# Optimization experiments

Hardware: AMD Instinct MI355X
Metric: run time of the kernel (lower is better)

Reference implementation:

```python
import jax, jax.numpy as jnp
import numpy as np

LEAKY = 0.1


def _leaky(x):
    return jnp.where(x > 0, x, LEAKY * x)


def _weightnet(d_xyz, ws):
    # d_xyz: [B,N,K,3]; ws: list of (w [Cin,Cout], b [Cout]) -> [B,N,K,W]
    h = d_xyz
    for w, b in ws:
        h = jax.nn.relu(jnp.einsum('bnki,io->bnko', h, w) + b)
    return h


def _gather(pts, idx):
    # pts: [B,M,C], idx: [B,N,K] -> [B,N,K,C]
    return jax.vmap(lambda p, i: p[i])(pts, idx)


def _cross(xyz1, xyz2, p1, p2, wn, lw, lb, nsample):
    # xyz1 [B,N1,3], xyz2 [B,N2,3], p1 [B,N1,D1], p2 [B,N2,D2]
    B, N1, _ = xyz1.shape
    # squared distances [B,N1,N2]
    d = (jnp.sum(xyz1 ** 2, -1)[:, :, None]
         + jnp.sum(xyz2 ** 2, -1)[:, None, :]
         - 2.0 * jnp.einsum('bnc,bmc->bnm', xyz1, xyz2))
    _, idx = jax.lax.top_k(-d, nsample)          # [B,N1,K] nearest
    neigh_xyz = _gather(xyz2, idx)               # [B,N1,K,3]
    direction = neigh_xyz - xyz1[:, :, None, :]  # [B,N1,K,3]
    gp2 = _gather(p2, idx)                       # [B,N1,K,D2]
    gp1 = jnp.broadcast_to(p1[:, :, None, :], (B, N1, nsample, p1.shape[-1]))
    new_pts = jnp.concatenate([gp1, gp2], axis=-1)   # [B,N1,K,D1+D2]
    w = _weightnet(direction, wn)                    # [B,N1,K,W]
    # [B,N1,D,K] @ [B,N1,K,W] -> [B,N1,D,W] -> flatten D-major (matches torch view)
    agg = jnp.einsum('bnkd,bnkw->bndw', new_pts, w).reshape(B, N1, -1)
    return _leaky(agg @ lw + lb)                     # [B,N1,out]


def setup_inputs() -> dict:
    key = jax.random.key(0)
    ks = jax.random.split(key, 20)
    B, N, C, MID, OUT, W = 4, 4096, 64, 128, 128, 16
    s = 0.05
    inp = {
        'pc1': jax.random.normal(ks[0], (B, 3, N), jnp.float32),
        'pc2': jax.random.normal(ks[1], (B, 3, N), jnp.float32),
        'feat1': jax.random.normal(ks[2], (B, C, N), jnp.float32),
        'feat2': jax.random.normal(ks[3], (B, C, N), jnp.float32),
        # WeightNet1: 3->8->8->16 pointwise linears (torch Conv2d 1x1), stored [Cin,Cout]
        'wn1_w0': jax.random.normal(ks[4], (3, 8), jnp.float32) * s,
        'wn1_b0': jnp.zeros((8,), jnp.float32),
        'wn1_w1': jax.random.normal(ks[5], (8, 8), jnp.float32) * s,
        'wn1_b1': jnp.zeros((8,), jnp.float32),
        'wn1_w2': jax.random.normal(ks[6], (8, W), jnp.float32) * s,
        'wn1_b2': jnp.zeros((W,), jnp.float32),
        'lin1_w': jax.random.normal(ks[7], (2 * C * W, MID), jnp.float32) * s,
        'lin1_b': jnp.zeros((MID,), jnp.float32),
        'wn2_w0': jax.random.normal(ks[8], (3, 8), jnp.float32) * s,
        'wn2_b0': jnp.zeros((8,), jnp.float32),
        'wn2_w1': jax.random.normal(ks[9], (8, 8), jnp.float32) * s,
        'wn2_b1': jnp.zeros((8,), jnp.float32),
        'wn2_w2': jax.random.normal(ks[10], (8, W), jnp.float32) * s,
        'wn2_b2': jnp.zeros((W,), jnp.float32),
        'lin2_w': jax.random.normal(ks[11], (2 * MID * W, OUT), jnp.float32) * s,
        'lin2_b': jnp.zeros((OUT,), jnp.float32),
    }
    return inp


def reference(pc1, pc2, feat1, feat2,
              wn1_w0, wn1_b0, wn1_w1, wn1_b1, wn1_w2, wn1_b2, lin1_w, lin1_b,
              wn2_w0, wn2_b0, wn2_w1, wn2_b1, wn2_w2, wn2_b2, lin2_w, lin2_b):
    nsample = 16
    wn1 = [(wn1_w0, wn1_b0), (wn1_w1, wn1_b1), (wn1_w2, wn1_b2)]
    wn2 = [(wn2_w0, wn2_b0), (wn2_w1, wn2_b1), (wn2_w2, wn2_b2)]
    x1 = pc1.transpose(0, 2, 1)   # [B,N,3]
    x2 = pc2.transpose(0, 2, 1)
    p1 = feat1.transpose(0, 2, 1)  # [B,N,C]
    p2 = feat2.transpose(0, 2, 1)
    f1n = _cross(x1, x2, p1, p2, wn1, lin1_w, lin1_b, nsample)   # [B,N1,mid]
    f2n = _cross(x2, x1, p2, p1, wn1, lin1_w, lin1_b, nsample)   # [B,N2,mid]
    f1f = _cross(x1, x2, f1n, f2n, wn2, lin2_w, lin2_b, nsample) # [B,N1,out]
    return (f1n.transpose(0, 2, 1), f2n.transpose(0, 2, 1), f1f.transpose(0, 2, 1))
```

## Files before the change

### kernel.cpp

```cpp
#include <hip/hip_runtime.h>
#include <hip/hip_bf16.h>
#include <cstddef>
#include <cstdint>

typedef __hip_bfloat16 bf16;
typedef __attribute__((ext_vector_type(8))) short bf16x8;
typedef __attribute__((ext_vector_type(4))) float f32x4;

#define NPT 4096
#define BB  4
#define NBR 16
#define WD  16
#define CDIM 64
#define MIDD 128

#define GLD16(g, l) __builtin_amdgcn_global_load_lds( \
    (const __attribute__((address_space(1))) unsigned int*)(const void*)(g), \
    (__attribute__((address_space(3))) unsigned int*)(void*)(l), 16, 0, 0)

#define KQ     16
#define KSEG   16
#define KCH    64
#define KSTAGE 1024
#define KRING  96

__global__ __launch_bounds__(256)
void pre_kernel(const float* __restrict__ pcA, const float* __restrict__ pcB,
                int* __restrict__ idxAB, int* __restrict__ idxBA,
                const float* __restrict__ feat1, const float* __restrict__ feat2,
                float* __restrict__ p1pm, bf16* __restrict__ p1b,
                float* __restrict__ p2pm, bf16* __restrict__ p2b,
                const float* __restrict__ lin1_w, bf16* __restrict__ b1hi, bf16* __restrict__ b1lo,
                const float* __restrict__ lin2_w, bf16* __restrict__ b2hi, bf16* __restrict__ b2lo)
{
    __shared__ float4 cf[KSTAGE + KSTAGE / KCH];
    __shared__ float  pubd[2][KSEG][KQ];
    __shared__ float4 qc[KQ];
    __shared__ float  u16s[KQ];
    __shared__ int    rcnt[KQ];
    __shared__ int    wtot;
    __shared__ int    wl[256];
    __shared__ float  ringd[KQ][KRING + 1];
    __shared__ int    ringi[KQ][KRING + 1];
    __shared__ float  t[32][33];

    const int bid = blockIdx.x;
    const int tid = threadIdx.x;

    if (bid < 2048) {
        const int dir = bid >> 10;
        const int b   = (bid >> 8) & 3;
        const int g   = bid & 255;
        const float* qxyz = dir ? pcB : pcA;
        const float* cxyz = dir ? pcA : pcB;
        int* idx_out      = dir ? idxBA : idxAB;

        const int q = tid & (KQ - 1);
        const int s = tid >> 4;
        const int n = g * KQ + q;

        const float* qp = qxyz + (size_t)b * 3 * NPT;
        const float qx = qp[n], qy = qp[NPT + n], qz = qp[2 * NPT + n];
        const float q2 = fmaf(qx, qx, fmaf(qy, qy, qz * qz));
        const float* c = cxyz + (size_t)b * 3 * NPT;

        if (tid < KQ) rcnt[tid] = 0;
        if (tid == 0) wtot = 0;
        if (s == 0) qc[q] = make_float4(qx, qy, qz, q2);

        float b0 = 3.4e38f, b1 = 3.4e38f;
        int   i0 = 0;
        for (int st = 0; st < NPT; st += KSTAGE) {
            __syncthreads();
            {
                #pragma unroll
                for (int r = 0; r < KSTAGE / 256; ++r) {
                    const int j = r * 256 + tid;
                    const int gg = st + j;
                    const float x = c[gg], y = c[NPT + gg], z = c[2 * NPT + gg];
                    cf[j + (j >> 6)] = make_float4(x, y, z,
                        fmaf(x, x, fmaf(y, y, z * z)));
                }
            }
            __syncthreads();
            const int base = s * (KCH + 1);
            const int gidx = st + s * KCH;
            #pragma unroll 4
            for (int jj = 0; jj < KCH; ++jj) {
                const float4 pv = cf[base + jj];
                const float dot = fmaf(qx, pv.x, fmaf(qy, pv.y, qz * pv.z));
                const float d = q2 + pv.w - 2.f * dot;
                i0 = (d < b0) ? (gidx + jj) : i0;
                const float tt = fmaxf(b0, d);
                b0 = fminf(b0, d);
                b1 = fminf(b1, tt);
            }
        }
        pubd[0][s][q] = b0;
        pubd[1][s][q] = b1;
        __syncthreads();

        {
            float tv[32];
            #pragma unroll
            for (int j = 0; j < 32; ++j) tv[j] = pubd[j >> 4][j & 15][q];
            #pragma unroll
            for (int rep = 0; rep < 2; ++rep) {
                const int j = rep * 16 + s;
                const float vj = pubd[rep][s][q];
                int rank = 0;
                #pragma unroll
                for (int k = 0; k < 32; ++k)
                    rank += (tv[k] < vj || (tv[k] == vj && k < j)) ? 1 : 0;
                if (rank == 15) u16s[q] = vj;
            }
        }
        __syncthreads();

        {
            const float gate = u16s[q];
            if (b0 <= gate) {
                if (b1 > gate) {
                    const int slot = atomicAdd(&rcnt[q], 1);
                    if (slot < KRING) { ringd[q][slot] = b0; ringi[q][slot] = i0; }
                } else {
                    const int u = atomicAdd(&wtot, 1);
                    wl[u] = (q << 4) | s;
                }
            }
        }
        __syncthreads();

        {
            const int W = wtot;
            const int lu = tid & 15;
            for (int u = tid >> 4; u < W; u += 16) {
                const int qq  = wl[u] >> 4;
                const int seg = wl[u] & 15;
                const float4 qv = qc[qq];
                const float gate = u16s[qq];
                #pragma unroll
                for (int ch = 0; ch < 4; ++ch) {
                    const int j = ch * KSTAGE + seg * KCH + lu * 4;
                    const float4 xs = *(const float4*)(c + j);
                    const float4 ys = *(const float4*)(c + NPT + j);
                    const float4 zs = *(const float4*)(c + 2 * NPT + j);
                    const float xv[4] = { xs.x, xs.y, xs.z, xs.w };
                    const float yv[4] = { ys.x, ys.y, ys.z, ys.w };
                    const float zv[4] = { zs.x, zs.y, zs.z, zs.w };
                    #pragma unroll
                    for (int e = 0; e < 4; ++e) {
                        const float p2 = fmaf(xv[e], xv[e], fmaf(yv[e], yv[e], zv[e] * zv[e]));
                        const float dot = fmaf(qv.x, xv[e], fmaf(qv.y, yv[e], qv.z * zv[e]));
                        const float d = qv.w + p2 - 2.f * dot;
                        if (d <= gate) {
                            const int slot = atomicAdd(&rcnt[qq], 1);
                            if (slot < KRING) { ringd[qq][slot] = d; ringi[qq][slot] = j + e; }
                        }
                    }
                }
            }
        }
        __syncthreads();

        {
            const int cnt = min(rcnt[q], KRING);
            int* op = idx_out + ((size_t)b * NPT + n) * NBR;
            for (int e = s; e < cnt; e += KSEG) {
                const float de = ringd[q][e];
                const int   ie = ringi[q][e];
                int rank = 0;
                for (int k = 0; k < cnt; ++k) {
                    const float dk = ringd[q][k];
                    const int   ik = ringi[q][k];
                    rank += (dk < de || (dk == de && ik < ie)) ? 1 : 0;
                }
                if (rank < NBR) op[rank] = ie;
            }
        }
    } else {
        const int tx = tid & 31, ty = tid >> 5;
        const int id = bid - 2048;
        if (id < 2048) {
            const int which = id >> 10;
            const int nt = id & 1023;
            const int n0 = (nt & 127) * 32;
            const int c0 = ((nt >> 7) & 1) * 32;
            const int b  = nt >> 8;
            const float* in = which ? feat2 : feat1;
            float* out  = which ? p2pm : p1pm;
            bf16*  outb = which ? p2b  : p1b;
            #pragma unroll
            for (int r = ty; r < 32; r += 8)
                t[r][tx] = in[((size_t)b * CDIM + c0 + r) * NPT + n0 + tx];
            __syncthreads();
            #pragma unroll
            for (int r = ty; r < 32; r += 8) {
                const float v = t[tx][r];
                out [((size_t)b * NPT + n0 + r) * CDIM + c0 + tx] = v;
                outb[((size_t)b * NPT + n0 + r) * CDIM + c0 + tx] = __float2bfloat16(v);
            }
        } else {
            const float* w; bf16 *hi, *lo; int K, k0, o0;
            if (id < 2304) {
                const int id2 = id - 2048;
                w = lin1_w; hi = b1hi; lo = b1lo; K = 2048;
                k0 = (id2 & 63) * 32; o0 = (id2 >> 6) * 32;
            } else {
                const int id2 = id - 2304;
                w = lin2_w; hi = b2hi; lo = b2lo; K = 4096;
                k0 = (id2 & 127) * 32; o0 = (id2 >> 7) * 32;
            }
            #pragma unroll
            for (int r = ty; r < 32; r += 8)
                t[r][tx] = w[(size_t)(k0 + r) * MIDD + o0 + tx];
            __syncthreads();
            #pragma unroll
            for (int r = ty; r < 32; r += 8) {
                const float v = t[tx][r];
                const bf16 h = __float2bfloat16(v);
                const bf16 l2 = __float2bfloat16(v - __bfloat162float(h));
                hi[(size_t)(o0 + r) * K + k0 + tx] = h;
                lo[(size_t)(o0 + r) * K + k0 + tx] = l2;
            }
        }
    }
}

template<int D2, int PTS>
__global__ __launch_bounds__(256)
void agg_kernel(const float* __restrict__ qA, const float* __restrict__ cA,
                const bf16* __restrict__ nbrA, const int* __restrict__ idxA,
                const float* __restrict__ qB, const float* __restrict__ cB,
                const bf16* __restrict__ nbrB, const int* __restrict__ idxB,
                int Msplit,
                const float* __restrict__ w0, const float* __restrict__ b0,
                const float* __restrict__ w1, const float* __restrict__ b1,
                const float* __restrict__ w2, const float* __restrict__ b2,
                bf16* __restrict__ agg, float* __restrict__ swb, int m0)
{
    constexpr int TPP  = 256 / PTS;
    constexpr int ND   = D2 / TPP;
    constexpr int WSTR = 276;

    __shared__ float wp[248];
    __shared__ int   nb[PTS * NBR];
    __shared__ float wgt[PTS * WSTR];

    const int tid = threadIdx.x;
    const int mbase = m0 + (int)blockIdx.x * PTS;
    const bool second = mbase >= Msplit;
    const int mrow = second ? mbase - Msplit : mbase;
    const float* qxyz   = second ? qB   : qA;
    const float* cxyz   = second ? cB   : cA;
    const bf16*  nbr_b  = second ? nbrB : nbrA;
    const int*   idx    = second ? idxB : idxA;
    const int b = mrow >> 12;
    const int nbase = mrow & (NPT - 1);

    if (tid < 248) {
        float v;
        if      (tid <  24) v = w0[tid];
        else if (tid <  32) v = b0[tid - 24];
        else if (tid <  96) v = w1[tid - 32];
        else if (tid < 104) v = b1[tid - 96];
        else if (tid < 232) v = w2[tid - 104];
        else                v = b2[tid - 232];
        wp[tid] = v;
    }
    if (tid < PTS * NBR)
        nb[tid] = idx[(size_t)mrow * NBR + tid];
    __syncthreads();

    const int p  = tid / TPP;
    const int dg = tid % TPP;
    const int d0 = dg * ND;

    unsigned int F[NBR];
    {
        const bf16* base = nbr_b + (size_t)b * NPT * D2 + d0;
        #pragma unroll
        for (int k = 0; k < NBR; ++k) {
            const int j = nb[p * NBR + k];
            F[k] = *(const unsigned int*)(base + (size_t)j * D2);
        }
    }

    if (tid < PTS * NBR) {
        const int pp = tid / NBR, k = tid % NBR;
        const int n = nbase + pp;
        const int j = nb[tid];
        const float* q = qxyz + (size_t)b * 3 * NPT;
        const float* c = cxyz + (size_t)b * 3 * NPT;
        const float dx = c[j]           - q[n];
        const float dy = c[NPT + j]     - q[NPT + n];
        const float dz = c[2 * NPT + j] - q[2 * NPT + n];
        float h1[8], h2[8];
        #pragma unroll
        for (int o = 0; o < 8; ++o) {
            float v = wp[24 + o];
            v = fmaf(dx, wp[o], v);
            v = fmaf(dy, wp[8 + o], v);
            v = fmaf(dz, wp[16 + o], v);
            h1[o] = fmaxf(v, 0.f);
        }
        #pragma unroll
        for (int o = 0; o < 8; ++o) {
            float v = wp[96 + o];
            #pragma unroll
            for (int i = 0; i < 8; ++i) v = fmaf(h1[i], wp[32 + i * 8 + o], v);
            h2[o] = fmaxf(v, 0.f);
        }
        #pragma unroll
        for (int o = 0; o < WD; ++o) {
            float v = wp[232 + o];
            #pragma unroll
            for (int i = 0; i < 8; ++i) v = fmaf(h2[i], wp[104 + i * WD + o], v);
            wgt[pp * WSTR + k * WD + o] = fmaxf(v, 0.f);
        }
    }
    __syncthreads();

    if (tid < PTS * 16) {
        const int pp = tid >> 4, w = tid & 15;
        const float* wgp = wgt + pp * WSTR + w;
        float sv = 0.f;
        #pragma unroll
        for (int k = 0; k < NBR; ++k) sv += wgp[k * WD];
        swb[(size_t)((int)blockIdx.x * PTS + pp) * 16 + w] = sv;
    }

    {
        const float* wg = wgt + p * WSTR;
        bf16* aout = agg + ((size_t)((int)blockIdx.x * PTS + p)) * (2 * D2 * WD);
        float acc[ND][16];
        #pragma unroll
        for (int di = 0; di < ND; ++di)
            #pragma unroll
            for (int w = 0; w < 16; ++w) acc[di][w] = 0.f;
        #pragma unroll
        for (int k = 0; k < NBR; ++k) {
            union { unsigned int u; bf16 h[2]; } uf;
            uf.u = F[k];
            float Fv[ND];
            #pragma unroll
            for (int j = 0; j < ND; ++j) Fv[j] = __bfloat162float(uf.h[j]);
            const float4 v0 = *(const float4*)(wg + k * WD);
            const float4 v1 = *(const float4*)(wg + k * WD + 4);
            const float4 v2 = *(const float4*)(wg + k * WD + 8);
            const float4 v3 = *(const float4*)(wg + k * WD + 12);
            float w16[16];
            w16[0]  = v0.x; w16[1]  = v0.y; w16[2]  = v0.z; w16[3]  = v0.w;
            w16[4]  = v1.x; w16[5]  = v1.y; w16[6]  = v1.z; w16[7]  = v1.w;
            w16[8]  = v2.x; w16[9]  = v2.y; w16[10] = v2.z; w16[11] = v2.w;
            w16[12] = v3.x; w16[13] = v3.y; w16[14] = v3.z; w16[15] = v3.w;
            #pragma unroll
            for (int di = 0; di < ND; ++di)
                #pragma unroll
                for (int w = 0; w < 16; ++w)
                    acc[di][w] = fmaf(Fv[di], w16[w], acc[di][w]);
        }
        #pragma unroll
        for (int di = 0; di < ND; ++di) {
            union { bf16 h[16]; uint4 q[2]; } pk;
            #pragma unroll
            for (int w = 0; w < 16; ++w) pk.h[w] = __float2bfloat16(acc[di][w]);
            bf16* dst = aout + (D2 + d0 + di) * WD;
            *(uint4*)dst       = pk.q[0];
            *(uint4*)(dst + 8) = pk.q[1];
        }
    }
}

template<int BM>
__global__ __launch_bounds__(256)
void gemm_mfma_k64(const bf16* __restrict__ A, const bf16* __restrict__ Bhi,
                   const bf16* __restrict__ Blo, const float* __restrict__ bias,
                   const float* __restrict__ ownf, const float* __restrict__ swb,
                   float* __restrict__ out_t, float* __restrict__ out_pm,
                   bf16* __restrict__ out_pmb, int m0, int K)
{
    constexpr int AE   = BM * 64;
    constexpr int BT   = 128 * 64;
    constexpr int BUFE = AE + 2 * BT;
    constexpr int MF   = BM / 32;
    constexpr int RA   = BM * 8 / 256;
    __shared__ __align__(16) char smem[2 * BUFE * 2];
    bf16* lds = (bf16*)smem;

    const int tid  = threadIdx.x;
    const int w    = tid >> 6;
    const int lane = tid & 63;
    const int wr   = w >> 1, wc = w & 1;
    const int mb   = (int)blockIdx.x * BM;
    const int gK   = lane >> 4;
    const int rL   = lane & 15;
    const int D2v  = K / 32;

    int rowA[RA], schA[RA];
    float sww[RA][8];
    const float* ownrow_g[RA];
    #pragma unroll
    for (int r = 0; r < RA; ++r) {
        const int slot = r * 256 + tid;
        rowA[r] = slot >> 3;
        const int ch = slot & 7;
        schA[r] = ch ^ (rowA[r] & 7);
        const int w0 = (schA[r] & 1) * 8;
        const float* sp = swb + (size_t)(mb + rowA[r]) * 16 + w0;
        const float4 a = *(const float4*)sp;
        const float4 b2 = *(const float4*)(sp + 4);
        sww[r][0] = a.x;  sww[r][1] = a.y;  sww[r][2] = a.z;  sww[r][3] = a.w;
        sww[r][4] = b2.x; sww[r][5] = b2.y; sww[r][6] = b2.z; sww[r][7] = b2.w;
        ownrow_g[r] = ownf + (size_t)(m0 + mb + rowA[r]) * D2v;
    }

    f32x4 acc[MF][4];
    #pragma unroll
    for (int i = 0; i < MF; ++i)
        #pragma unroll
        for (int j = 0; j < 4; ++j) acc[i][j] = (f32x4)0.f;

    const int nk = K / 64;
    const int nkOwn = nk / 2;

    auto stage = [&](int buf, int kt) {
        const int kb = kt * 64;
        const int bufo = buf * BUFE;
        if (kt < nkOwn) {
            #pragma unroll
            for (int r = 0; r < RA; ++r) {
                const int d = kt * 4 + (schA[r] >> 1);
                const float f = ownrow_g[r][d];
                union { bf16 h[8]; uint4 q; } pk;
                #pragma unroll
                for (int j = 0; j < 8; ++j) pk.h[j] = __float2bfloat16(f * sww[r][j]);
                *(uint4*)(lds + bufo + (r * 256 + tid) * 8) = pk.q;
            }
        } else {
            #pragma unroll
            for (int r = 0; r < RA; ++r)
                GLD16(A + (size_t)(mb + rowA[r]) * K + kb + (schA[r] << 3),
                      lds + bufo + ((r * 256 + w * 64) << 3));
        }
        #pragma unroll
        for (int i = 0; i < 4; ++i) {
            const int s2 = i * 256 + tid;
            const int row = s2 >> 3, ch = s2 & 7;
            const int sch = ch ^ (row & 7);
            const int wb = (i * 256 + w * 64) << 3;
            GLD16(Bhi + (size_t)row * K + kb + (sch << 3), lds + bufo + AE + wb);
            GLD16(Blo + (size_t)row * K + kb + (sch << 3), lds + bufo + AE + BT + wb);
        }
    };

    stage(0, 0);
    __syncthreads();

    for (int kt = 0; kt < nk; ++kt) {
        const int cur = kt & 1;
        if (kt + 1 < nk) stage(cur ^ 1, kt + 1);

        const bf16* la  = lds + cur * BUFE;
        const bf16* lbh = la + AE;
        const bf16* lbl = la + AE + BT;

        #pragma unroll
        for (int kk2 = 0; kk2 < 2; ++kk2) {
            const int cc = gK + kk2 * 4;
            bf16x8 af[MF], bh[4], bl[4];
            #pragma unroll
            for (int mf = 0; mf < MF; ++mf) {
                const int row = wr * (BM / 2) + mf * 16 + rL;
                af[mf] = *(const bf16x8*)(la + row * 64 + ((cc ^ (row & 7)) << 3));
            }
            #pragma unroll
            for (int nf = 0; nf < 4; ++nf) {
                const int col = wc * 64 + nf * 16 + rL;
                const int off = col * 64 + ((cc ^ (col & 7)) << 3);
                bh[nf] = *(const bf16x8*)(lbh + off);
                bl[nf] = *(const bf16x8*)(lbl + off);
            }
            #pragma unroll
            for (int mf = 0; mf < MF; ++mf)
                #pragma unroll
                for (int nf = 0; nf < 4; ++nf) {
                    acc[mf][nf] = __builtin_amdgcn_mfma_f32_16x16x32_bf16(af[mf], bh[nf], acc[mf][nf], 0, 0, 0);
                    acc[mf][nf] = __builtin_amdgcn_mfma_f32_16x16x32_bf16(af[mf], bl[nf], acc[mf][nf], 0, 0, 0);
                }
        }
        __syncthreads();
    }

    float (*tile)[133] = (float(*)[133])smem;
    #pragma unroll
    for (int mf = 0; mf < MF; ++mf)
        #pragma unroll
        for (int nf = 0; nf < 4; ++nf) {
            const int col = wc * 64 + nf * 16 + rL;
            const float bs = bias[col];
            #pragma unroll
            for (int qq = 0; qq < 4; ++qq) {
                const int rrow = wr * (BM / 2) + mf * 16 + gK * 4 + qq;
                const float v = acc[mf][nf][qq] + bs;
                tile[rrow][col] = v > 0.f ? v : 0.1f * v;
            }
        }
    __syncthreads();

    const int mrow = m0 + mb;
    const int b = mrow >> 12, n0 = mrow & (NPT - 1);
    for (int e = tid; e < BM * MIDD; e += 256) {
        const int o = e / BM, i = e % BM;
        out_t[((size_t)b * MIDD + o) * NPT + n0 + i] = tile[i][o];
    }
    if (out_pm) {
        for (int e = tid; e < BM * MIDD; e += 256) {
            const int i = e >> 7, o = e & 127;
            const float v = tile[i][o];
            out_pm [(size_t)(mrow + i) * MIDD + o] = v;
            out_pmb[(size_t)(mrow + i) * MIDD + o] = __float2bfloat16(v);
        }
    }
}

extern "C" void kernel_launch(void* const* d_in, const int* in_sizes, int n_in,
                              void* d_out, int out_size, void* d_ws, size_t ws_size,
                              hipStream_t stream)
{
    (void)in_sizes; (void)n_in; (void)out_size;
    const float* pc1    = (const float*)d_in[0];
    const float* pc2    = (const float*)d_in[1];
    const float* feat1  = (const float*)d_in[2];
    const float* feat2  = (const float*)d_in[3];
    const float* wn1_w0 = (const float*)d_in[4];
    const float* wn1_b0 = (const float*)d_in[5];
    const float* wn1_w1 = (const float*)d_in[6];
    const float* wn1_b1 = (const float*)d_in[7];
    const float* wn1_w2 = (const float*)d_in[8];
    const float* wn1_b2 = (const float*)d_in[9];
    const float* lin1_w = (const float*)d_in[10];
    const float* lin1_b = (const float*)d_in[11];
    const float* wn2_w0 = (const float*)d_in[12];
    const float* wn2_b0 = (const float*)d_in[13];
    const float* wn2_w1 = (const float*)d_in[14];
    const float* wn2_b1 = (const float*)d_in[15];
    const float* wn2_w2 = (const float*)d_in[16];
    const float* wn2_b2 = (const float*)d_in[17];
    const float* lin2_w = (const float*)d_in[18];
    const float* lin2_b = (const float*)d_in[19];
    float* out = (float*)d_out;

    const int M  = BB * NPT;
    const int M2 = 2 * M;
    const int K1 = 2 * CDIM * WD;
    const int K2 = 2 * MIDD * WD;

    char* ws = (char*)d_ws;
    float* p1pm = (float*)ws;
    float* p2pm = p1pm + (size_t)M * CDIM;
    float* fpm  = p2pm + (size_t)M * CDIM;
    bf16*  p1b  = (bf16*)(fpm + (size_t)M2 * MIDD);
    bf16*  p2b  = p1b + (size_t)M * CDIM;
    bf16*  fb   = p2b + (size_t)M * CDIM;
    int* idx12  = (int*)(fb + (size_t)M2 * MIDD);
    int* idx21  = idx12 + (size_t)M * NBR;
    bf16* b1hi  = (bf16*)(idx21 + (size_t)M * NBR);
    bf16* b1lo  = b1hi + (size_t)MIDD * K1;
    bf16* b2hi  = b1lo + (size_t)MIDD * K1;
    bf16* b2lo  = b2hi + (size_t)MIDD * K2;
    float* swbuf = (float*)(b2lo + (size_t)MIDD * K2);
    bf16* aggbuf = (bf16*)(swbuf + (size_t)(M2 + 64) * 16);
    const size_t used = (size_t)((char*)aggbuf - ws);
    const size_t avail = ws_size > used ? ws_size - used : 0;

    float* f1t = out;
    float* fft = out + 2 * (size_t)BB * MIDD * NPT;

    pre_kernel<<<2048 + 2816, 256, 0, stream>>>(
        pc1, pc2, idx12, idx21,
        feat1, feat2, p1pm, p1b, p2pm, p2b,
        lin1_w, b1hi, b1lo, lin2_w, b2hi, b2lo);

    auto chunk_rows = [&](int K) -> int {
        long rows = (long)(avail / ((size_t)K * sizeof(bf16)));
        int cm = (int)(rows > M2 ? M2 : rows) & ~127;
        if (cm < 128) cm = 128;
        return cm;
    };

    {
        const int CMr = chunk_rows(K1);
        for (int m0 = 0; m0 < M2; m0 += CMr) {
            const int cm = (M2 - m0 < CMr) ? (M2 - m0) : CMr;
            agg_kernel<CDIM, 8><<<cm / 8, 256, 0, stream>>>(
                pc1, pc2, p2b, idx12,
                pc2, pc1, p1b, idx21, M,
                wn1_w0, wn1_b0, wn1_w1, wn1_b1, wn1_w2, wn1_b2,
                aggbuf, swbuf, m0);
            gemm_mfma_k64<64><<<cm / 64, 256, 0, stream>>>(aggbuf, b1hi, b1lo, lin1_b,
                                                           p1pm, swbuf,
                                                           f1t, fpm, fb, m0, K1);
        }
    }
    {
        const int CMr = chunk_rows(K2);
        for (int m0 = 0; m0 < M; m0 += CMr) {
            const int cm = (M - m0 < CMr) ? (M - m0) : CMr;
            agg_kernel<MIDD, 4><<<cm / 4, 256, 0, stream>>>(
                pc1, pc2, fb + (size_t)M * MIDD, idx12,
                nullptr, nullptr, nullptr, nullptr, M2,
                wn2_w0, wn2_b0, wn2_w1, wn2_b1, wn2_w2, wn2_b2,
                aggbuf, swbuf, m0);
            gemm_mfma_k64<32><<<cm / 32, 256, 0, stream>>>(aggbuf, b2hi, b2lo, lin2_b,
                                                           fpm, swbuf,
                                                           fft, nullptr, nullptr, m0, K2);
        }
    }
}
```

Baseline: 269.0 us.

## Stream candidate coords from global in kNN, cache only norms in LDS; split pm writes

The kNN scan no longer stages full float4 candidate points through LDS in four barrier-separated stages. It precomputes all candidate squared norms into LDS once, then reads x/y/z straight from global memory with float4 loads, four candidates per iteration. Separately, the GEMM epilogue now writes the fp32 pointwise output only for rows of the first cloud and the bf16 copy only for rows of the second. This assumes the later stages consume only those halves, which is a correctness risk if not true. The kNN change removes barriers and LDS staging but relies on cache hits for the repeated global coordinate reads.

```diff
diff --git a/kernel.cpp b/kernel.cpp
--- a/kernel.cpp
+++ b/kernel.cpp
@@ -33,7 +33,7 @@
                 const float* __restrict__ lin1_w, bf16* __restrict__ b1hi, bf16* __restrict__ b1lo,
                 const float* __restrict__ lin2_w, bf16* __restrict__ b2hi, bf16* __restrict__ b2lo)
 {
-    __shared__ float4 cf[KSTAGE + KSTAGE / KCH];
+    __shared__ float  p2s[NPT + 256];
     __shared__ float  pubd[2][KSEG][KQ];
     __shared__ float4 qc[KQ];
     __shared__ float  u16s[KQ];
@@ -68,32 +68,39 @@
         if (tid == 0) wtot = 0;
         if (s == 0) qc[q] = make_float4(qx, qy, qz, q2);
 
+        #pragma unroll
+        for (int r = 0; r < NPT / 256; ++r) {
+            const int j = r * 256 + tid;
+            const float x = c[j], y = c[NPT + j], z = c[2 * NPT + j];
+            p2s[j + ((j >> 6) << 2)] = fmaf(x, x, fmaf(y, y, z * z));
+        }
+        __syncthreads();
+
         float b0 = 3.4e38f, b1 = 3.4e38f;
         int   i0 = 0;
-        for (int st = 0; st < NPT; st += KSTAGE) {
-            __syncthreads();
-            {
+        #pragma unroll 1
+        for (int ch = 0; ch < 4; ++ch) {
+            const int segbase = ch * KSTAGE + s * KCH;
+            #pragma unroll 4
+            for (int jj = 0; jj < KCH; jj += 4) {
+                const int j = segbase + jj;
+                const float4 xs = *(const float4*)(c + j);
+                const float4 ys = *(const float4*)(c + NPT + j);
+                const float4 zs = *(const float4*)(c + 2 * NPT + j);
+                const float4 ps = *(const float4*)&p2s[j + ((j >> 6) << 2)];
+                const float xv[4] = { xs.x, xs.y, xs.z, xs.w };
+                const float yv[4] = { ys.x, ys.y, ys.z, ys.w };
+                const float zv[4] = { zs.x, zs.y, zs.z, zs.w };
+                const float pv[4] = { ps.x, ps.y, ps.z, ps.w };
                 #pragma unroll
-                for (int r = 0; r < KSTAGE / 256; ++r) {
-                    const int j = r * 256 + tid;
-                    const int gg = st + j;
-                    const float x = c[gg], y = c[NPT + gg], z = c[2 * NPT + gg];
-                    cf[j + (j >> 6)] = make_float4(x, y, z,
-                        fmaf(x, x, fmaf(y, y, z * z)));
+                for (int e = 0; e < 4; ++e) {
+                    const float dot = fmaf(qx, xv[e], fmaf(qy, yv[e], qz * zv[e]));
+                    const float d = q2 + pv[e] - 2.f * dot;
+                    i0 = (d < b0) ? (j + e) : i0;
+                    const float tt = fmaxf(b0, d);
+                    b0 = fminf(b0, d);
+                    b1 = fminf(b1, tt);
                 }
-            }
-            __syncthreads();
-            const int base = s * (KCH + 1);
-            const int gidx = st + s * KCH;
-            #pragma unroll 4
-            for (int jj = 0; jj < KCH; ++jj) {
-                const float4 pv = cf[base + jj];
-                const float dot = fmaf(qx, pv.x, fmaf(qy, pv.y, qz * pv.z));
-                const float d = q2 + pv.w - 2.f * dot;
-                i0 = (d < b0) ? (gidx + jj) : i0;
-                const float tt = fmaxf(b0, d);
-                b0 = fminf(b0, d);
-                b1 = fminf(b1, tt);
             }
         }
         pubd[0][s][q] = b0;
@@ -378,7 +385,7 @@
                    const bf16* __restrict__ Blo, const float* __restrict__ bias,
                    const float* __restrict__ ownf, const float* __restrict__ swb,
                    float* __restrict__ out_t, float* __restrict__ out_pm,
-                   bf16* __restrict__ out_pmb, int m0, int K)
+                   bf16* __restrict__ out_pmb, int Msplit, int m0, int K)
 {
     constexpr int AE   = BM * 64;
     constexpr int BT   = 128 * 64;
@@ -514,12 +521,16 @@
         const int o = e / BM, i = e % BM;
         out_t[((size_t)b * MIDD + o) * NPT + n0 + i] = tile[i][o];
     }
-    if (out_pm) {
+    if (out_pm && mrow < Msplit) {
         for (int e = tid; e < BM * MIDD; e += 256) {
             const int i = e >> 7, o = e & 127;
-            const float v = tile[i][o];
-            out_pm [(size_t)(mrow + i) * MIDD + o] = v;
-            out_pmb[(size_t)(mrow + i) * MIDD + o] = __float2bfloat16(v);
+            out_pm[(size_t)(mrow + i) * MIDD + o] = tile[i][o];
+        }
+    }
+    if (out_pmb && mrow >= Msplit) {
+        for (int e = tid; e < BM * MIDD; e += 256) {
+            const int i = e >> 7, o = e & 127;
+            out_pmb[(size_t)(mrow + i) * MIDD + o] = __float2bfloat16(tile[i][o]);
         }
     }
 }
@@ -600,7 +611,7 @@
                 aggbuf, swbuf, m0);
             gemm_mfma_k64<64><<<cm / 64, 256, 0, stream>>>(aggbuf, b1hi, b1lo, lin1_b,
                                                            p1pm, swbuf,
-                                                           f1t, fpm, fb, m0, K1);
+                                                           f1t, fpm, fb, M, m0, K1);
         }
     }
     {
@@ -614,7 +625,7 @@
                 aggbuf, swbuf, m0);
             gemm_mfma_k64<32><<<cm / 32, 256, 0, stream>>>(aggbuf, b2hi, b2lo, lin2_b,
                                                            fpm, swbuf,
-                                                           fft, nullptr, nullptr, m0, K2);
+                                                           fft, nullptr, nullptr, 0, m0, K2);
         }
     }
 }
```

After: 279.3 us. +3.8%, slower.
